# Kernel optimization log

Hardware: AMD Instinct MI355X
Metric: run time of the kernel (lower is better)

The kernel has to match this reference:

```python
import jax, jax.numpy as jnp
import numpy as np

B, T, D, H, C = 256, 256, 512, 1024, 128  # batch, steps, input_size, hidden, num_classes


def setup_inputs() -> dict:
    key = jax.random.key(0)
    ks = jax.random.split(key, 8)
    gru_inputs = jax.random.normal(ks[0], (B, T, D), dtype=jnp.float32)
    true_ids = jax.random.randint(ks[1], (B, T), 0, C)
    true_seq = jax.nn.one_hot(true_ids, C, dtype=jnp.float32)
    s = 1.0 / np.sqrt(H).astype(np.float32)
    W_ih = jax.random.uniform(ks[2], (3 * H, D + C), jnp.float32, -s, s)
    b_ih = jax.random.uniform(ks[3], (3 * H,), jnp.float32, -s, s)
    W_hh = jax.random.uniform(ks[4], (3 * H, H), jnp.float32, -s, s)
    b_hh = jax.random.uniform(ks[5], (3 * H,), jnp.float32, -s, s)
    W_out = jax.random.uniform(ks[6], (C, H), jnp.float32, -s, s)
    b_out = jax.random.uniform(ks[7], (C,), jnp.float32, -s, s)
    return {"gru_inputs": gru_inputs, "true_seq": true_seq, "W_ih": W_ih,
            "b_ih": b_ih, "W_hh": W_hh, "b_hh": b_hh, "W_out": W_out, "b_out": b_out}


def reference(gru_inputs, true_seq, W_ih, b_ih, W_hh, b_hh, W_out, b_out):
    # Teacher-forcing (training) branch of TerminalGRU, dropout=0, bos_idx=None.
    Bb, Tt, _ = gru_inputs.shape
    Cc = true_seq.shape[-1]
    Hh = W_hh.shape[1]
    # prev_y[t] = true_seq[t-1], prev_y[0] = zeros (no BOS)
    prev_y = jnp.concatenate(
        [jnp.zeros((Bb, 1, Cc), gru_inputs.dtype), true_seq[:, :-1]], axis=1)
    inp = jnp.concatenate([gru_inputs, prev_y], axis=-1)  # (B,T,D+C)
    # Precompute input-side gate projections as one big GEMM (faithful math).
    gates_x = jnp.einsum('btd,gd->btg', inp, W_ih) + b_ih  # (B,T,3H)
    xr, xz, xn = jnp.split(gates_x, 3, axis=-1)

    def step(h, xs):
        xr_t, xz_t, xn_t = xs  # each (B,H)
        gh = h @ W_hh.T + b_hh  # (B,3H)
        hr, hz, hn = jnp.split(gh, 3, axis=-1)
        r = jax.nn.sigmoid(xr_t + hr)
        z = jax.nn.sigmoid(xz_t + hz)
        n = jnp.tanh(xn_t + r * hn)
        h_new = (1.0 - z) * n + z * h
        return h_new, h_new

    h0 = jnp.zeros((Bb, Hh), gru_inputs.dtype)
    xs = (xr.transpose(1, 0, 2), xz.transpose(1, 0, 2), xn.transpose(1, 0, 2))
    _, hs = jax.lax.scan(step, h0, xs)  # hs: (T,B,H)
    logits = jnp.einsum('tbh,ch->btc', hs, W_out) + b_out  # (B,T,C)
    return logits
```

## Files before the change

### kernel.cpp

```cpp
#include <hip/hip_runtime.h>


#define DEVI __device__ __forceinline__

typedef __bf16 bf16x8 __attribute__((ext_vector_type(8)));
typedef float f32x4 __attribute__((ext_vector_type(4)));
typedef unsigned long long u64;

static constexpr int Bb = 256, Tt = 256, Dd = 512, Hh = 1024, Cc = 128;
static constexpr int G3 = 3072, DC = 640, TC = 32, NC = Tt / TC;
static constexpr int SLOTS = TC + 1;

DEVI unsigned short f2b(float f) {
  union { float f; unsigned u; } v; v.f = f;
  unsigned r = v.u + 0x7FFFu + ((v.u >> 16) & 1u);
  return (unsigned short)(r >> 16);
}
DEVI float b2f(unsigned short h) {
  union { unsigned u; float f; } v; v.u = ((unsigned)h) << 16; return v.f;
}

DEVI void gload16(const unsigned short* g, unsigned short* l) {
  __builtin_amdgcn_global_load_lds(
      (const __attribute__((address_space(1))) unsigned int*)g,
      (__attribute__((address_space(3))) unsigned int*)l, 16, 0, 0);
}


__global__ __launch_bounds__(256) void k_cvt(const float* __restrict__ x,
                                             unsigned short* __restrict__ o, int n) {
  int i = (blockIdx.x * 256 + threadIdx.x) * 8;
  if (i >= n) return;
  float4 a = *(const float4*)(x + i), b = *(const float4*)(x + i + 4);
  uint4 u;
  u.x = (unsigned)f2b(a.x) | ((unsigned)f2b(a.y) << 16);
  u.y = (unsigned)f2b(a.z) | ((unsigned)f2b(a.w) << 16);
  u.z = (unsigned)f2b(b.x) | ((unsigned)f2b(b.y) << 16);
  u.w = (unsigned)f2b(b.z) | ((unsigned)f2b(b.w) << 16);
  *(uint4*)(o + i) = u;
}

__global__ __launch_bounds__(256) void k_cvt_wa(const float* __restrict__ Wih,
                                                unsigned short* __restrict__ Wa) {
  int u = blockIdx.x * 256 + threadIdx.x;
  int g = u >> 6, d = (u & 63) * 8;
  const float* p = Wih + (size_t)g * DC + d;
  float4 a = *(const float4*)p, b = *(const float4*)(p + 4);
  uint4 o;
  o.x = (unsigned)f2b(a.x) | ((unsigned)f2b(a.y) << 16);
  o.y = (unsigned)f2b(a.z) | ((unsigned)f2b(a.w) << 16);
  o.z = (unsigned)f2b(b.x) | ((unsigned)f2b(b.y) << 16);
  o.w = (unsigned)f2b(b.z) | ((unsigned)f2b(b.w) << 16);
  *(uint4*)(Wa + (size_t)g * Dd + d) = o;
}

__global__ __launch_bounds__(256) void k_cvt_wct(const float* __restrict__ Wih,
                                                 unsigned short* __restrict__ WcT) {
  int g = blockIdx.x * 256 + threadIdx.x;
  int c = blockIdx.y;
  WcT[(size_t)c * G3 + g] = f2b(Wih[(size_t)g * DC + Dd + c]);
}

__global__ __launch_bounds__(256) void k_pid(const float* __restrict__ ts,
                                             int* __restrict__ pid) {
  int bt = blockIdx.x * 256 + threadIdx.x;
  int t = bt & (Tt - 1);
  if (t == 0) { pid[bt] = -1; return; }
  const float* p = ts + (size_t)(bt - 1) * Cc;
  int id = 0;
  for (int c = 0; c < Cc; c += 4) {
    float4 v = *(const float4*)(p + c);
    if (v.x > 0.5f) id = c;
    if (v.y > 0.5f) id = c + 1;
    if (v.z > 0.5f) id = c + 2;
    if (v.w > 0.5f) id = c + 3;
  }
  pid[bt] = id;
}

DEVI void gates_tile(int mi, int ni, const unsigned short* __restrict__ Xb,
                     const unsigned short* __restrict__ Wa,
                     const unsigned short* __restrict__ WcT,
                     const float* __restrict__ bih,
                     const int* __restrict__ pid,
                     unsigned short* __restrict__ gx, int t0c,
                     unsigned short* sA, unsigned short* sB) {
  const int m0 = mi * 128, n0 = ni * 128;
  const int tid = threadIdx.x;
  const int l = tid & 63, w = tid >> 6;
  const int wm = w >> 1, wn = w & 1;
  const int r0l = 64 * wm, c0l = 64 * wn;
  const int lr = l & 15, lk = (l >> 4) * 8;

  const unsigned short* gsrc[4];
  unsigned short* ldst[4];
#pragma unroll
  for (int p = 0; p < 4; ++p) {
    int slot = p * 256 + tid;
    if (slot < 512) {
      int row = slot >> 2, q = slot & 3;
      int mrow = m0 + row;
      gsrc[p] = Xb + ((size_t)((mrow >> 5) * Tt + t0c + (mrow & 31))) * Dd + q * 8;
      ldst[p] = sA + (size_t)(p * 256 + 64 * w) * 8;
    } else {
      int s2 = slot - 512;
      int row = s2 >> 2, q = s2 & 3;
      gsrc[p] = Wa + (size_t)(n0 + row) * Dd + q * 8;
      ldst[p] = sB + (size_t)((p - 2) * 256 + 64 * w) * 8;
    }
  }

  f32x4 acc[4][4] = {};
  for (int ks = 0; ks < 16; ++ks) {
    int k0 = ks * 32;
    __syncthreads();
#pragma unroll
    for (int p = 0; p < 4; ++p)
      gload16(gsrc[p] + k0, ldst[p]);
    __syncthreads();
    bf16x8 a[4], b[4];
#pragma unroll
    for (int mf = 0; mf < 4; ++mf)
      a[mf] = *(const bf16x8*)(sA + (r0l + 16 * mf + lr) * 32 + lk);
#pragma unroll
    for (int nf = 0; nf < 4; ++nf)
      b[nf] = *(const bf16x8*)(sB + (c0l + 16 * nf + lr) * 32 + lk);
#pragma unroll
    for (int mf = 0; mf < 4; ++mf)
#pragma unroll
      for (int nf = 0; nf < 4; ++nf)
        acc[mf][nf] = __builtin_amdgcn_mfma_f32_16x16x32_bf16(a[mf], b[nf], acc[mf][nf], 0, 0, 0);
  }

  const int ri = (l >> 4) * 4;
  const int r0 = m0 + 64 * wm, c0 = n0 + 64 * wn;
  for (int mf = 0; mf < 4; ++mf) {
    int rowb = r0 + 16 * mf + ri;
    int pd[4];
#pragma unroll
    for (int i = 0; i < 4; ++i) {
      int rr = rowb + i;
      pd[i] = pid[(size_t)(rr >> 5) * Tt + t0c + (rr & 31)];
    }
    for (int nf = 0; nf < 4; ++nf) {
      int g = c0 + 16 * nf + lr;
      float bi = bih[g];
#pragma unroll
      for (int i = 0; i < 4; ++i) {
        float v = acc[mf][nf][i] + bi;
        if (pd[i] >= 0) v += b2f(WcT[(size_t)pd[i] * G3 + g]);
        gx[(size_t)(rowb + i) * G3 + g] = f2b(v);
      }
    }
  }
}

__global__ __launch_bounds__(256) void k_gates(const unsigned short* __restrict__ Xb,
                                               const unsigned short* __restrict__ Wa,
                                               const unsigned short* __restrict__ WcT,
                                               const float* __restrict__ bih,
                                               const int* __restrict__ pid,
                                               unsigned short* __restrict__ gx, int t0c) {
  __shared__ unsigned short sA[128 * 32], sB[128 * 32];
  gates_tile(blockIdx.x, blockIdx.y, Xb, Wa, WcT, bih, pid, gx, t0c, sA, sB);
}

DEVI void logits_tile(int blk, const unsigned short* __restrict__ hring,
                      const unsigned short* __restrict__ Wo,
                      const float* __restrict__ bout,
                      float* __restrict__ out, int t0) {
  int l = threadIdx.x & 63, w = threadIdx.x >> 6;
  int lr = l & 15, lk = (l >> 4) * 8;
  int r0 = blk * 64 + 16 * w;
  int am = r0 + lr;
  int ab = am >> 5, atl = am & 31;
  const unsigned short* arow =
      hring + (size_t)((t0 + atl + 1) % SLOTS) * (Bb * Hh) + (size_t)ab * Hh;
  f32x4 acc[8] = {};
  for (int kk = 0; kk < 32; ++kk) {
    int k = kk * 32 + lk;
    bf16x8 a = *(const bf16x8*)(arow + k);
#pragma unroll
    for (int nf = 0; nf < 8; ++nf) {
      bf16x8 b = *(const bf16x8*)(Wo + (size_t)(16 * nf + lr) * Hh + k);
      acc[nf] = __builtin_amdgcn_mfma_f32_16x16x32_bf16(a, b, acc[nf], 0, 0, 0);
    }
  }
  int ri = (l >> 4) * 4;
  for (int nf = 0; nf < 8; ++nf) {
    int c = 16 * nf + lr;
    float bo = bout[c];
#pragma unroll
    for (int i = 0; i < 4; ++i) {
      int m = r0 + ri + i;
      int grow = (m >> 5) * Tt + t0 + (m & 31);
      out[(size_t)grow * Cc + c] = acc[nf][i] + bo;
    }
  }
}

__global__ __launch_bounds__(256) void k_combo(
    const unsigned short* __restrict__ Xb, const unsigned short* __restrict__ Wa,
    const unsigned short* __restrict__ WcT, const float* __restrict__ bih,
    const int* __restrict__ pid, unsigned short* __restrict__ gxNext, int doGates,
    const unsigned short* __restrict__ hring, const unsigned short* __restrict__ Wob,
    const float* __restrict__ bou, float* __restrict__ outp, int t0) {
  __shared__ unsigned short sA[128 * 32], sB[128 * 32];
  int bid = blockIdx.x;
  if (bid < 1536) {
    if (doGates)
      gates_tile(bid & 63, bid >> 6, Xb, Wa, WcT, bih, pid, gxNext, t0 + TC, sA, sB);
  } else {
    logits_tile(bid - 1536, hring, Wob, bou, outp, t0);
  }
}

__global__ __launch_bounds__(256, 1) void k_scan(const unsigned short* __restrict__ Whh,
                                                 const float* __restrict__ bhh,
                                                 const unsigned short* __restrict__ gx,
                                                 unsigned short* __restrict__ hring,
                                                 unsigned int* __restrict__ notify,
                                                 int t0) {
  __shared__ float red[4 * 32 * 100];
  const int tid = threadIdx.x;
  const int l = tid & 63, w = tid >> 6;
  const int bid = blockIdx.x;
  const int mg = bid & 7, cb = bid >> 3;
  const int lr = l & 15, lk = (l >> 4) * 8;
  const int hcolBase = 32 * cb;
  const int ri = (l >> 4) * 4;

  bf16x8 Breg[6][8];
#pragma unroll
  for (int nf = 0; nf < 6; ++nf) {
    int wrow = (nf >> 1) * Hh + hcolBase + (nf & 1) * 16 + lr;
#pragma unroll
    for (int kk = 0; kk < 8; ++kk) {
      int k = 256 * w + 32 * kk + lk;
      Breg[nf][kk] = *(const bf16x8*)(Whh + (size_t)wrow * Hh + k);
    }
  }

  const int erow = tid >> 3, ej0 = (tid & 7) * 4;
  const int eb = 32 * mg + erow;
  const int ecol = hcolBase + ej0;
  const float4 bhr4 = *(const float4*)(bhh + ecol);
  const float4 bhz4 = *(const float4*)(bhh + Hh + ecol);
  const float4 bhn4 = *(const float4*)(bhh + 2 * Hh + ecol);

  u64 hsave = 0;

  for (int tl = 0; tl < TC; ++tl) {
    const int t = t0 + tl;
    const unsigned short* hcur = hring + (size_t)(t % SLOTS) * (Bb * Hh);
    u64* hnq = (u64*)hring + (size_t)((t + 1) % SLOTS) * (Bb * Hh / 4);

    const size_t gxo = (size_t)(eb * TC + tl) * G3;
    uint2 gr = *(const uint2*)(gx + gxo + ecol);
    uint2 gz = *(const uint2*)(gx + gxo + Hh + ecol);
    uint2 gn = *(const uint2*)(gx + gxo + 2 * Hh + ecol);

    if (t > 0) {
      const unsigned int* np = notify + (mg << 6) + 8 * w + (l & 7);
      for (;;) {
        unsigned int v = __hip_atomic_load(np, __ATOMIC_RELAXED,
                                           __HIP_MEMORY_SCOPE_AGENT);
        if (__all((int)(v >= (unsigned)t))) break;
      }
    }
    asm volatile("" ::: "memory");

    u64 hprev = (tl == 0) ? *(const u64*)(hcur + (size_t)eb * Hh + ecol) : hsave;

    f32x4 acc[2][6] = {};
#pragma unroll
    for (int kk = 0; kk < 8; ++kk) {
      int k = 256 * w + 32 * kk + lk;
      bf16x8 a[2];
#pragma unroll
      for (int mf = 0; mf < 2; ++mf)
        a[mf] = *(const bf16x8*)(hcur + (size_t)(32 * mg + 16 * mf + lr) * Hh + k);
#pragma unroll
      for (int mf = 0; mf < 2; ++mf)
#pragma unroll
        for (int nf = 0; nf < 6; ++nf)
          acc[mf][nf] = __builtin_amdgcn_mfma_f32_16x16x32_bf16(a[mf], Breg[nf][kk], acc[mf][nf], 0, 0, 0);
    }

#pragma unroll
    for (int mf = 0; mf < 2; ++mf)
#pragma unroll
      for (int nf = 0; nf < 6; ++nf)
#pragma unroll
        for (int i = 0; i < 4; ++i)
          red[(w * 32 + 16 * mf + ri + i) * 100 + (nf >> 1) * 32 + (nf & 1) * 16 + lr] = acc[mf][nf][i];
    __syncthreads();

    f32x4 vr = {}, vz = {}, vn = {};
#pragma unroll
    for (int w2 = 0; w2 < 4; ++w2) {
      const float* rp = &red[(w2 * 32 + erow) * 100];
      vr += *(const f32x4*)(rp + ej0);
      vz += *(const f32x4*)(rp + 32 + ej0);
      vn += *(const f32x4*)(rp + 64 + ej0);
    }
    unsigned short grs[4] = {(unsigned short)gr.x, (unsigned short)(gr.x >> 16),
                             (unsigned short)gr.y, (unsigned short)(gr.y >> 16)};
    unsigned short gzs[4] = {(unsigned short)gz.x, (unsigned short)(gz.x >> 16),
                             (unsigned short)gz.y, (unsigned short)(gz.y >> 16)};
    unsigned short gns[4] = {(unsigned short)gn.x, (unsigned short)(gn.x >> 16),
                             (unsigned short)gn.y, (unsigned short)(gn.y >> 16)};
    u64 ho = 0;
#pragma unroll
    for (int i = 0; i < 4; ++i) {
      float hr = vr[i] + (&bhr4.x)[i];
      float hz = vz[i] + (&bhz4.x)[i];
      float hn = vn[i] + (&bhn4.x)[i];
      float xr = b2f(grs[i]), xz = b2f(gzs[i]), xn = b2f(gns[i]);
      float rg = 1.f / (1.f + __expf(-(xr + hr)));
      float zg = 1.f / (1.f + __expf(-(xz + hz)));
      float pre = xn + rg * hn;
      pre = fminf(fmaxf(pre, -15.f), 15.f);
      float e = __expf(-2.f * pre);
      float ng = (1.f - e) / (1.f + e);
      float hp = b2f((unsigned short)(hprev >> (16 * i)));
      float hv = (1.f - zg) * ng + zg * hp;
      ho |= (u64)f2b(hv) << (16 * i);
    }
    __hip_atomic_store(hnq + ((size_t)eb * Hh + ecol) / 4, ho,
                       __ATOMIC_RELAXED, __HIP_MEMORY_SCOPE_AGENT);
    hsave = ho;

    asm volatile("s_waitcnt vmcnt(0)" ::: "memory");
    __syncthreads();
    if (tid == 0)
      __hip_atomic_store(notify + (mg << 6) + cb, (unsigned)(t + 1),
                         __ATOMIC_RELAXED, __HIP_MEMORY_SCOPE_AGENT);
  }
}

extern "C" void kernel_launch(void* const* d_in, const int* in_sizes, int n_in,
                              void* d_out, int out_size, void* d_ws, size_t ws_size,
                              hipStream_t stream) {
  const float* gru = (const float*)d_in[0];
  const float* ts  = (const float*)d_in[1];
  const float* Wih = (const float*)d_in[2];
  const float* bih = (const float*)d_in[3];
  const float* Whh = (const float*)d_in[4];
  const float* bhh = (const float*)d_in[5];
  const float* Wou = (const float*)d_in[6];
  const float* bou = (const float*)d_in[7];
  float* out = (float*)d_out;

  char* ws = (char*)d_ws;
  size_t off = 0;
  auto alloc = [&](size_t bytes) -> void* {
    void* p = ws + off;
    off += (bytes + 255) & ~(size_t)255;
    return p;
  };
  unsigned short* Wa    = (unsigned short*)alloc((size_t)G3 * Dd * 2);
  unsigned short* WcT   = (unsigned short*)alloc((size_t)Cc * G3 * 2);
  unsigned short* Whb   = (unsigned short*)alloc((size_t)G3 * Hh * 2);
  unsigned short* Wob   = (unsigned short*)alloc((size_t)Cc * Hh * 2);
  int*            pid   = (int*)alloc((size_t)Bb * Tt * 4);
  unsigned short* hring = (unsigned short*)alloc((size_t)SLOTS * Bb * Hh * 2);
  unsigned int*   nfy   = (unsigned int*)alloc((size_t)8 * 64 * 4);
  unsigned short* Xb    = (unsigned short*)alloc((size_t)Bb * Tt * Dd * 2);
  unsigned short* gx    = (unsigned short*)alloc((size_t)Bb * TC * G3 * 2);
  if (ws_size < off) return;

  int nX = Bb * Tt * Dd;
  k_cvt<<<nX / 2048, 256, 0, stream>>>(gru, Xb, nX);
  k_cvt<<<(G3 * Hh) / 2048, 256, 0, stream>>>(Whh, Whb, G3 * Hh);
  k_cvt<<<(Cc * Hh) / 2048, 256, 0, stream>>>(Wou, Wob, Cc * Hh);
  k_cvt_wa<<<(G3 * 64) / 256, 256, 0, stream>>>(Wih, Wa);
  k_cvt_wct<<<dim3(G3 / 256, Cc), 256, 0, stream>>>(Wih, WcT);
  k_pid<<<(Bb * Tt) / 256, 256, 0, stream>>>(ts, pid);
  hipMemsetAsync(hring, 0, (size_t)Bb * Hh * 2, stream);
  hipMemsetAsync(nfy, 0, (size_t)8 * 64 * 4, stream);

  k_gates<<<dim3(64, 24), 256, 0, stream>>>(Xb, Wa, WcT, bih, pid, gx, 0);

  for (int c = 0; c < NC; ++c) {
    int t0 = c * TC;
    k_scan<<<dim3(256), dim3(256), 0, stream>>>(Whb, bhh, gx, hring, nfy, t0);
    k_combo<<<dim3(1664), dim3(256), 0, stream>>>(
        Xb, Wa, WcT, bih, pid, gx, (c + 1 < NC) ? 1 : 0,
        hring, Wob, bou, out, t0);
  }
}
```

Measured before the change: 2.274 ms.

## Fuse gate projection and logits work into the persistent scan kernel

Removes the separate combo kernel launched after each scan chunk. Each scan block first waits until every block in its batch group has finished the chunk. It then computes six gate-projection tiles for the next chunk and, for half of the blocks, one logits tile. The goal is to save a launch per chunk and let groups that finish early start their follow-up work while others are still scanning. The trade-off is that this GEMM work now runs on only 256 blocks at one block per CU with a large LDS footprint. That means less latency hiding than the old 1664-block launch had. The gx buffer is also overwritten within the same kernel that read it, which relies on the group-wise wait for correctness.

```diff
diff --git a/kernel.cpp b/kernel.cpp
--- a/kernel.cpp
+++ b/kernel.cpp
@@ -199,29 +199,17 @@
   }
 }
 
-__global__ __launch_bounds__(256) void k_combo(
+__global__ __launch_bounds__(256, 1) void k_scan(
+    const unsigned short* __restrict__ Whh, const float* __restrict__ bhh,
+    const unsigned short* __restrict__ gx, unsigned short* __restrict__ hring,
+    unsigned int* __restrict__ notify, int t0,
     const unsigned short* __restrict__ Xb, const unsigned short* __restrict__ Wa,
     const unsigned short* __restrict__ WcT, const float* __restrict__ bih,
-    const int* __restrict__ pid, unsigned short* __restrict__ gxNext, int doGates,
-    const unsigned short* __restrict__ hring, const unsigned short* __restrict__ Wob,
-    const float* __restrict__ bou, float* __restrict__ outp, int t0) {
+    const int* __restrict__ pid, unsigned short* __restrict__ gxw, int doGates,
+    const unsigned short* __restrict__ Wob, const float* __restrict__ bou,
+    float* __restrict__ outp) {
+  __shared__ float red[4 * 32 * 100];
   __shared__ unsigned short sA[128 * 32], sB[128 * 32];
-  int bid = blockIdx.x;
-  if (bid < 1536) {
-    if (doGates)
-      gates_tile(bid & 63, bid >> 6, Xb, Wa, WcT, bih, pid, gxNext, t0 + TC, sA, sB);
-  } else {
-    logits_tile(bid - 1536, hring, Wob, bou, outp, t0);
-  }
-}
-
-__global__ __launch_bounds__(256, 1) void k_scan(const unsigned short* __restrict__ Whh,
-                                                 const float* __restrict__ bhh,
-                                                 const unsigned short* __restrict__ gx,
-                                                 unsigned short* __restrict__ hring,
-                                                 unsigned int* __restrict__ notify,
-                                                 int t0) {
-  __shared__ float red[4 * 32 * 100];
   const int tid = threadIdx.x;
   const int l = tid & 63, w = tid >> 6;
   const int bid = blockIdx.x;
@@ -337,6 +325,27 @@
       __hip_atomic_store(notify + (mg << 6) + cb, (unsigned)(t + 1),
                          __ATOMIC_RELAXED, __HIP_MEMORY_SCOPE_AGENT);
   }
+
+  {
+    const unsigned int* np = notify + (mg << 6) + (l & 31);
+    for (;;) {
+      unsigned int v = __hip_atomic_load(np, __ATOMIC_RELAXED,
+                                         __HIP_MEMORY_SCOPE_AGENT);
+      if (__all((int)(v >= (unsigned)(t0 + TC)))) break;
+    }
+  }
+  asm volatile("" ::: "memory");
+
+  if (doGates) {
+    for (int j = 0; j < 6; ++j) {
+      int tau = cb * 6 + j;
+      gates_tile(8 * mg + (tau / 24), tau % 24, Xb, Wa, WcT, bih, pid,
+                 gxw, t0 + TC, sA, sB);
+    }
+  }
+
+  if (cb < 16)
+    logits_tile(16 * mg + cb, hring, Wob, bou, outp, t0);
 }
 
 extern "C" void kernel_launch(void* const* d_in, const int* in_sizes, int n_in,
@@ -384,9 +393,9 @@
 
   for (int c = 0; c < NC; ++c) {
     int t0 = c * TC;
-    k_scan<<<dim3(256), dim3(256), 0, stream>>>(Whb, bhh, gx, hring, nfy, t0);
-    k_combo<<<dim3(1664), dim3(256), 0, stream>>>(
+    k_scan<<<dim3(256), dim3(256), 0, stream>>>(
+        Whb, bhh, gx, hring, nfy, t0,
         Xb, Wa, WcT, bih, pid, gx, (c + 1 < NC) ? 1 : 0,
-        hring, Wob, bou, out, t0);
-  }
-}
+        Wob, bou, out);
+  }
+}
```

New measurement: 2.492 ms. 9.6% more time.
